# Performance work log

Hardware: AMD Instinct MI355X
Metric: run time of the kernel (lower is better)

## Reference

```python
import jax, jax.numpy as jnp
import numpy as np

N_HEADS = 16

def setup_inputs() -> dict:
    key = jax.random.key(0)
    k1, k2, k3 = jax.random.split(key, 3)
    B, T, C = 4, 2048, 1024
    x = jax.random.normal(k1, (B, T, C), dtype=jnp.float32)
    W_kqv = jax.random.normal(k2, (C, 3 * C), dtype=jnp.float32) * (C ** -0.5)
    W_proj = jax.random.normal(k3, (C, C), dtype=jnp.float32) * (C ** -0.5)
    return {"x": x, "W_kqv": W_kqv, "W_proj": W_proj}


def reference(x, W_kqv, W_proj):
    # x: (B,T,C). Dropout layers are identity in eval mode (p treated as 0).
    B, T, C = x.shape
    H = N_HEADS
    D = C // H
    dk = D ** -0.5
    kqv = x @ W_kqv                     # (B,T,3C)
    kqv = kqv.reshape(B, T, 3, H, D).transpose(2, 0, 3, 1, 4)  # (3,B,H,T,D)
    k, q, v = kqv[0], kqv[1], kqv[2]    # note: k first, matching source
    scores = jnp.einsum('bhqd,bhkd->bhqk', q, k) * dk  # (B,H,T,T)
    attn = jax.nn.softmax(scores, axis=-1)
    out = jnp.einsum('bhqk,bhkd->bhqd', attn, v)       # (B,H,T,D)
    out = out.transpose(0, 2, 1, 3).reshape(B, T, C)   # (B,T,C)
    return out @ W_proj
```

## Files before the change

### kernel.cpp

```cpp
#include <hip/hip_runtime.h>
#include <hip/hip_bf16.h>

typedef unsigned short ushort_t;
typedef __attribute__((ext_vector_type(8))) short short8;
typedef __attribute__((ext_vector_type(4))) float f32x4;

__device__ __forceinline__ ushort_t f2bf(float f) {
    union { float f; unsigned int u; } v; v.f = f;
    unsigned int r = v.u + 0x7fffu + ((v.u >> 16) & 1u);
    return (ushort_t)(r >> 16);
}

__device__ __forceinline__ unsigned int cvtpk(float lo, float hi) {
    unsigned int r;
    asm("v_cvt_pk_bf16_f32 %0, %1, %2" : "=v"(r) : "v"(lo), "v"(hi));
    return r;
}

__device__ __forceinline__ void async16(const ushort_t* g, ushort_t* l) {
    __builtin_amdgcn_global_load_lds((const __attribute__((address_space(1))) void*)g,
                                     (__attribute__((address_space(3))) void*)l,
                                     16, 0, 0);
}

__global__ void cvt_bf16(const float* __restrict__ src, ushort_t* __restrict__ dst) {
    int i = (blockIdx.x * 256 + threadIdx.x) * 8;
    float4 f0 = *(const float4*)(src + i);
    float4 f1 = *(const float4*)(src + i + 4);
    union { uint4 v; ushort_t e[8]; } d;
    d.e[0]=f2bf(f0.x); d.e[1]=f2bf(f0.y); d.e[2]=f2bf(f0.z); d.e[3]=f2bf(f0.w);
    d.e[4]=f2bf(f1.x); d.e[5]=f2bf(f1.y); d.e[6]=f2bf(f1.z); d.e[7]=f2bf(f1.w);
    *(uint4*)(dst + i) = d.v;
}

__global__ void transpose_w(const float* __restrict__ src, ushort_t* __restrict__ dst,
                            int R, int C) {
    __shared__ ushort_t tile[32][33];
    const int bx = blockIdx.x * 32, by = blockIdx.y * 32;
    const int tx = threadIdx.x, ty = threadIdx.y;
    #pragma unroll
    for (int i = 0; i < 32; i += 8)
        tile[ty + i][tx] = f2bf(src[(size_t)(by + ty + i) * C + bx + tx]);
    __syncthreads();
    #pragma unroll
    for (int i = 0; i < 32; i += 8)
        dst[(size_t)(bx + ty + i) * R + by + tx] = tile[tx][ty + i];
}

__global__ void transpose_v(const ushort_t* __restrict__ kqv, ushort_t* __restrict__ vT) {
    __shared__ ushort_t tile[32][33];
    const int bh = blockIdx.z;
    const int b = bh >> 4, h = bh & 15;
    const int t0 = blockIdx.x * 32, d0 = blockIdx.y * 32;
    const int tx = threadIdx.x, ty = threadIdx.y;
    #pragma unroll
    for (int i = 0; i < 32; i += 8)
        tile[ty + i][tx] = kqv[(size_t)(b * 2048 + t0 + ty + i) * 3072 + 2048 + h * 64 + d0 + tx];
    __syncthreads();
    #pragma unroll
    for (int i = 0; i < 32; i += 8)
        vT[((size_t)bh * 64 + d0 + ty + i) * 2048 + t0 + tx] = tile[tx][ty + i];
}

template <bool CF32>
__global__ __launch_bounds__(256, 2)
void gemm_bt(const ushort_t* __restrict__ A, const ushort_t* __restrict__ Bt,
             void* __restrict__ Cv, int M, int N, int K) {
    constexpr int BK = 32;
    __shared__ ushort_t As[128 * BK];
    __shared__ ushort_t Bs[128 * BK];

    const int tid  = threadIdx.x;
    const int wave = tid >> 6;
    const int lane = tid & 63;
    const int quad = lane >> 4;
    const int l16  = lane & 15;
    const int m0 = blockIdx.x * 128;
    const int n0 = blockIdx.y * 128;
    const int wm = (wave >> 1) * 64;
    const int wn = (wave & 1) * 64;
    const int rA = (lane >> 2);
    const int cA = (lane & 3) * 8;

    f32x4 acc[4][4] = {};

    for (int k0 = 0; k0 < K; k0 += BK) {
        __syncthreads();
        #pragma unroll
        for (int u = 0; u < 2; ++u) {
            int c = wave * 2 + u;
            int row = c * 16 + rA;
            async16(A  + (size_t)(m0 + row) * K + k0 + cA, As + c * 512);
            async16(Bt + (size_t)(n0 + row) * K + k0 + cA, Bs + c * 512);
        }
        __syncthreads();

        short8 af[4], bf[4];
        #pragma unroll
        for (int mt = 0; mt < 4; ++mt)
            af[mt] = *(const short8*)(As + (wm + mt * 16 + l16) * BK + quad * 8);
        #pragma unroll
        for (int nt = 0; nt < 4; ++nt)
            bf[nt] = *(const short8*)(Bs + (wn + nt * 16 + l16) * BK + quad * 8);

        #pragma unroll
        for (int mt = 0; mt < 4; ++mt)
            #pragma unroll
            for (int nt = 0; nt < 4; ++nt)
                acc[mt][nt] = __builtin_amdgcn_mfma_f32_16x16x32_bf16(
                    af[mt], bf[nt], acc[mt][nt], 0, 0, 0);
    }

    #pragma unroll
    for (int mt = 0; mt < 4; ++mt) {
        #pragma unroll
        for (int r = 0; r < 4; ++r) {
            int row = m0 + wm + mt * 16 + quad * 4 + r;
            if constexpr (CF32) {
                float* op = (float*)Cv + (size_t)row * N + n0 + wn + l16;
                #pragma unroll
                for (int nt = 0; nt < 4; ++nt) op[nt * 16] = acc[mt][nt][r];
            } else {
                ushort_t* op = (ushort_t*)Cv + (size_t)row * N + n0 + wn + l16;
                #pragma unroll
                for (int nt = 0; nt < 4; ++nt) op[nt * 16] = f2bf(acc[mt][nt][r]);
            }
        }
    }
}

__global__ __launch_bounds__(256, 3)
void attn_kernel(const ushort_t* __restrict__ kqv, const ushort_t* __restrict__ vT,
                 ushort_t* __restrict__ aout) {
    constexpr int T = 2048;
    constexpr float SC = 0.18033688011112042f;

    __shared__ __align__(16) ushort_t smem[16384];
    ushort_t* Ks = smem;
    ushort_t* Vs = smem + 4096;
    ushort_t* Ps = smem + 8192;

    const int tid  = threadIdx.x;
    const int wave = tid >> 6;
    const int lane = tid & 63;
    const int quad = lane >> 4;
    const int l16  = lane & 15;

    const int lin = blockIdx.x;
    const int qt  = (lin >> 3) & 15;
    const int bh  = ((lin >> 7) << 3) | (lin & 7);
    const int b   = bh >> 4, h = bh & 15;
    const int q0  = qt * 128;
    const size_t rowBase = (size_t)b * T;

    short8 qf[2][2];
    #pragma unroll
    for (int mt = 0; mt < 2; ++mt) {
        const ushort_t* qp = kqv + (rowBase + q0 + wave * 32 + mt * 16 + l16) * 3072 + 1024 + h * 64;
        qf[mt][0] = *(const short8*)(qp + quad * 8);
        qf[mt][1] = *(const short8*)(qp + 32 + quad * 8);
    }

    const ushort_t* kbase = kqv + rowBase * 3072 + h * 64;
    const ushort_t* vbase = vT + (size_t)bh * 64 * 2048;
    ushort_t* pw = Ps + wave * 2048;

    const int swz = l16 & 7;
    const int qh  = quad >> 1;
    int wrow[2], gxo[4];
    #pragma unroll
    for (int mt = 0; mt < 2; ++mt) wrow[mt] = (mt * 16 + l16) * 64 + (quad & 1) * 4;
    #pragma unroll
    for (int nt = 0; nt < 4; ++nt) gxo[nt] = ((nt * 2 + qh) ^ swz) * 8;

    f32x4 O[2][4] = {};
    float lrow[2] = {};

    for (int kk = 0; kk < T; kk += 64) {
        __syncthreads();
        #pragma unroll
        for (int u = 0; u < 2; ++u) {
            int g = u * 256 + tid;
            int row = g >> 3, pos = g & 7;
            int c = pos ^ (row & 7);
            async16(kbase + (size_t)(kk + row) * 3072 + c * 8, Ks + g * 8);
            async16(vbase + (size_t)row * 2048 + kk + c * 8, Vs + g * 8);
        }
        __syncthreads();

        f32x4 S[2][4];
        #pragma unroll
        for (int nt = 0; nt < 4; ++nt) {
            int key = nt * 16 + l16;
            const ushort_t* kr = Ks + key * 64;
            short8 kf0 = *(const short8*)(kr + ((quad     ^ (l16 & 7)) * 8));
            short8 kf1 = *(const short8*)(kr + (((quad+4) ^ (l16 & 7)) * 8));
            #pragma unroll
            for (int mt = 0; mt < 2; ++mt) {
                f32x4 s = {0.f, 0.f, 0.f, 0.f};
                s = __builtin_amdgcn_mfma_f32_16x16x32_bf16(kf0, qf[mt][0], s, 0, 0, 0);
                s = __builtin_amdgcn_mfma_f32_16x16x32_bf16(kf1, qf[mt][1], s, 0, 0, 0);
                S[mt][nt] = s;
            }
        }

        #pragma unroll
        for (int mt = 0; mt < 2; ++mt) {
            #pragma unroll
            for (int nt = 0; nt < 4; ++nt) {
                float p0 = __builtin_amdgcn_exp2f(S[mt][nt][0] * SC);
                float p1 = __builtin_amdgcn_exp2f(S[mt][nt][1] * SC);
                float p2 = __builtin_amdgcn_exp2f(S[mt][nt][2] * SC);
                float p3 = __builtin_amdgcn_exp2f(S[mt][nt][3] * SC);
                lrow[mt] += (p0 + p1) + (p2 + p3);
                uint2 w;
                w.x = cvtpk(p0, p1);
                w.y = cvtpk(p2, p3);
                *(uint2*)(pw + wrow[mt] + gxo[nt]) = w;
            }
        }
        asm volatile("s_waitcnt lgkmcnt(0)" ::: "memory");

        short8 pf[2][2];
        #pragma unroll
        for (int mt = 0; mt < 2; ++mt)
            #pragma unroll
            for (int f = 0; f < 2; ++f)
                pf[mt][f] = *(const short8*)(pw + (mt * 16 + l16) * 64 + (((f * 4 + quad) ^ swz) * 8));

        #pragma unroll
        for (int dt = 0; dt < 4; ++dt) {
            int d = dt * 16 + l16;
            const ushort_t* vr = Vs + d * 64;
            short8 vf0 = *(const short8*)(vr + ((quad     ^ (l16 & 7)) * 8));
            short8 vf1 = *(const short8*)(vr + (((quad+4) ^ (l16 & 7)) * 8));
            #pragma unroll
            for (int mt = 0; mt < 2; ++mt) {
                O[mt][dt] = __builtin_amdgcn_mfma_f32_16x16x32_bf16(pf[mt][0], vf0, O[mt][dt], 0, 0, 0);
                O[mt][dt] = __builtin_amdgcn_mfma_f32_16x16x32_bf16(pf[mt][1], vf1, O[mt][dt], 0, 0, 0);
            }
        }
    }

    #pragma unroll
    for (int mt = 0; mt < 2; ++mt) {
        float s = lrow[mt];
        s += __shfl_xor(s, 16, 64);
        s += __shfl_xor(s, 32, 64);
        float inv[4];
        #pragma unroll
        for (int r = 0; r < 4; ++r)
            inv[r] = 1.f / __shfl(s, quad * 4 + r, 64);
        #pragma unroll
        for (int dt = 0; dt < 4; ++dt)
            #pragma unroll
            for (int r = 0; r < 4; ++r) {
                int row = q0 + wave * 32 + mt * 16 + quad * 4 + r;
                aout[(rowBase + row) * 1024 + h * 64 + dt * 16 + l16] = f2bf(O[mt][dt][r] * inv[r]);
            }
    }
}

extern "C" void kernel_launch(void* const* d_in, const int* in_sizes, int n_in,
                              void* d_out, int out_size, void* d_ws, size_t ws_size,
                              hipStream_t stream) {
    const float* x     = (const float*)d_in[0];
    const float* Wkqv  = (const float*)d_in[1];
    const float* Wproj = (const float*)d_in[2];
    float* out = (float*)d_out;

    constexpr int M = 8192, K = 1024;
    char* ws = (char*)d_ws;
    ushort_t* kqv    = (ushort_t*)(ws);
    ushort_t* vT     = (ushort_t*)(ws + 50331648);
    ushort_t* xb     = (ushort_t*)(ws + 67108864);
    ushort_t* aout   = xb;
    ushort_t* WkqvT  = (ushort_t*)(ws + 83886080);
    ushort_t* WprojT = (ushort_t*)(ws + 90177536);

    cvt_bf16<<<4096, 256, 0, stream>>>(x, xb);
    transpose_w<<<dim3(96, 32), dim3(32, 8), 0, stream>>>(Wkqv, WkqvT, 1024, 3072);
    transpose_w<<<dim3(32, 32), dim3(32, 8), 0, stream>>>(Wproj, WprojT, 1024, 1024);

    gemm_bt<false><<<dim3(M / 128, 3072 / 128), 256, 0, stream>>>(xb, WkqvT, kqv, M, 3072, K);
    transpose_v<<<dim3(64, 2, 64), dim3(32, 8), 0, stream>>>(kqv, vT);
    attn_kernel<<<1024, 256, 0, stream>>>(kqv, vT, aout);
    gemm_bt<true><<<dim3(M / 128, 1024 / 128), 256, 0, stream>>>(aout, WprojT, out, M, 1024, K);
}
```

Measured before the change: 273.7 us.

## Double-buffer K/V tiles in attention and fold softmax scale into Q weights

The attention kernel now keeps two shared-memory buffers for K and V and prefetches the next tile asynchronously while the current one is being computed. It waits only on the older loads (vmcnt(4)), so global-load latency overlaps with the MFMA and exp work. The softmax scale (dk times log2 e) is folded into the Q columns of W_kqv when that weight is converted, which removes a multiply per score element. The extra buffer raises LDS use from 32KB to 48KB per block, which may cut occupancy against the launch bounds of 3 blocks per CU. Scaling before the bf16 rounding slightly changes numerics.

```diff
diff --git a/kernel.cpp b/kernel.cpp
--- a/kernel.cpp
+++ b/kernel.cpp
@@ -34,13 +34,14 @@
 }
 
 __global__ void transpose_w(const float* __restrict__ src, ushort_t* __restrict__ dst,
-                            int R, int C) {
+                            int R, int C, int lo, int hi, float scale) {
     __shared__ ushort_t tile[32][33];
     const int bx = blockIdx.x * 32, by = blockIdx.y * 32;
     const int tx = threadIdx.x, ty = threadIdx.y;
+    const float s = (bx + tx >= lo && bx + tx < hi) ? scale : 1.0f;
     #pragma unroll
     for (int i = 0; i < 32; i += 8)
-        tile[ty + i][tx] = f2bf(src[(size_t)(by + ty + i) * C + bx + tx]);
+        tile[ty + i][tx] = f2bf(src[(size_t)(by + ty + i) * C + bx + tx] * s);
     __syncthreads();
     #pragma unroll
     for (int i = 0; i < 32; i += 8)
@@ -133,12 +134,10 @@
 void attn_kernel(const ushort_t* __restrict__ kqv, const ushort_t* __restrict__ vT,
                  ushort_t* __restrict__ aout) {
     constexpr int T = 2048;
-    constexpr float SC = 0.18033688011112042f;
-
-    __shared__ __align__(16) ushort_t smem[16384];
-    ushort_t* Ks = smem;
-    ushort_t* Vs = smem + 4096;
-    ushort_t* Ps = smem + 8192;
+    constexpr int NT = T / 64;
+
+    __shared__ __align__(16) ushort_t smem[24576];
+    ushort_t* const Ps = smem + 16384;
 
     const int tid  = threadIdx.x;
     const int wave = tid >> 6;
@@ -163,7 +162,7 @@
 
     const ushort_t* kbase = kqv + rowBase * 3072 + h * 64;
     const ushort_t* vbase = vT + (size_t)bh * 64 * 2048;
-    ushort_t* pw = Ps + wave * 2048;
+    ushort_t* const pw = Ps + wave * 2048;
 
     const int swz = l16 & 7;
     const int qh  = quad >> 1;
@@ -173,20 +172,37 @@
     #pragma unroll
     for (int nt = 0; nt < 4; ++nt) gxo[nt] = ((nt * 2 + qh) ^ swz) * 8;
 
-    f32x4 O[2][4] = {};
-    float lrow[2] = {};
-
-    for (int kk = 0; kk < T; kk += 64) {
-        __syncthreads();
+    auto stage = [&](ushort_t* dk, ushort_t* dv, int kk) {
         #pragma unroll
         for (int u = 0; u < 2; ++u) {
             int g = u * 256 + tid;
             int row = g >> 3, pos = g & 7;
             int c = pos ^ (row & 7);
-            async16(kbase + (size_t)(kk + row) * 3072 + c * 8, Ks + g * 8);
-            async16(vbase + (size_t)row * 2048 + kk + c * 8, Vs + g * 8);
-        }
-        __syncthreads();
+            async16(kbase + (size_t)(kk + row) * 3072 + c * 8, dk + g * 8);
+            async16(vbase + (size_t)row * 2048 + kk + c * 8, dv + g * 8);
+        }
+    };
+
+    f32x4 O[2][4] = {};
+    float lrow[2] = {};
+
+    stage(smem, smem + 4096, 0);
+
+    #pragma unroll 2
+    for (int t = 0; t < NT; ++t) {
+        ushort_t* const Ks = smem + ((t & 1) << 13);
+        ushort_t* const Vs = Ks + 4096;
+        ushort_t* const Kn = smem + (((t & 1) ^ 1) << 13);
+
+        __builtin_amdgcn_s_barrier();
+        if (t + 1 < NT) {
+            stage(Kn, Kn + 4096, (t + 1) * 64);
+            asm volatile("s_waitcnt vmcnt(4)" ::: "memory");
+        } else {
+            asm volatile("s_waitcnt vmcnt(0)" ::: "memory");
+        }
+        __builtin_amdgcn_s_barrier();
+        __builtin_amdgcn_sched_barrier(0);
 
         f32x4 S[2][4];
         #pragma unroll
@@ -208,10 +224,10 @@
         for (int mt = 0; mt < 2; ++mt) {
             #pragma unroll
             for (int nt = 0; nt < 4; ++nt) {
-                float p0 = __builtin_amdgcn_exp2f(S[mt][nt][0] * SC);
-                float p1 = __builtin_amdgcn_exp2f(S[mt][nt][1] * SC);
-                float p2 = __builtin_amdgcn_exp2f(S[mt][nt][2] * SC);
-                float p3 = __builtin_amdgcn_exp2f(S[mt][nt][3] * SC);
+                float p0 = __builtin_amdgcn_exp2f(S[mt][nt][0]);
+                float p1 = __builtin_amdgcn_exp2f(S[mt][nt][1]);
+                float p2 = __builtin_amdgcn_exp2f(S[mt][nt][2]);
+                float p3 = __builtin_amdgcn_exp2f(S[mt][nt][3]);
                 lrow[mt] += (p0 + p1) + (p2 + p3);
                 uint2 w;
                 w.x = cvtpk(p0, p1);
@@ -270,6 +286,7 @@
     float* out = (float*)d_out;
 
     constexpr int M = 8192, K = 1024;
+    constexpr float SC = 0.18033688011112042f;
     char* ws = (char*)d_ws;
     ushort_t* kqv    = (ushort_t*)(ws);
     ushort_t* vT     = (ushort_t*)(ws + 50331648);
@@ -279,8 +296,8 @@
     ushort_t* WprojT = (ushort_t*)(ws + 90177536);
 
     cvt_bf16<<<4096, 256, 0, stream>>>(x, xb);
-    transpose_w<<<dim3(96, 32), dim3(32, 8), 0, stream>>>(Wkqv, WkqvT, 1024, 3072);
-    transpose_w<<<dim3(32, 32), dim3(32, 8), 0, stream>>>(Wproj, WprojT, 1024, 1024);
+    transpose_w<<<dim3(96, 32), dim3(32, 8), 0, stream>>>(Wkqv, WkqvT, 1024, 3072, 1024, 2048, SC);
+    transpose_w<<<dim3(32, 32), dim3(32, 8), 0, stream>>>(Wproj, WprojT, 1024, 1024, 0, 0, 1.0f);
 
     gemm_bt<false><<<dim3(M / 128, 3072 / 128), 256, 0, stream>>>(xb, WkqvT, kqv, M, 3072, K);
     transpose_v<<<dim3(64, 2, 64), dim3(32, 8), 0, stream>>>(kqv, vT);
```

Result: faster. 267.3 us (-2.3%).
